# Kernel tuning notes

Hardware: AMD Instinct MI355X
Metric: run time of the kernel (lower is better)

The kernel has to match this reference:

```python
import jax, jax.numpy as jnp
import numpy as np

B, S, D, H = 4, 2048, 1024, 16
HD = D // H

def setup_inputs() -> dict:
    key = jax.random.key(0)
    ks = jax.random.split(key, 5)
    scale = 1.0 / np.sqrt(D)
    x = jax.random.normal(ks[0], (B, S, D), dtype=jnp.float32)
    Wq = jax.random.uniform(ks[1], (D, D), dtype=jnp.float32, minval=-scale, maxval=scale)
    Wk = jax.random.uniform(ks[2], (D, D), dtype=jnp.float32, minval=-scale, maxval=scale)
    Wv = jax.random.uniform(ks[3], (D, D), dtype=jnp.float32, minval=-scale, maxval=scale)
    Wo = jax.random.uniform(ks[4], (D, D), dtype=jnp.float32, minval=-scale, maxval=scale)
    return {"x": x, "Wq": Wq, "Wk": Wk, "Wv": Wv, "Wo": Wo}

def reference(x, Wq, Wk, Wv, Wo):
    # q/k/v: [B,S,D] @ [D,D] -> [B,S,H,HD] -> [B,H,S,HD]
    def heads(w):
        return (x @ w.T).reshape(B, S, H, HD).transpose(0, 2, 1, 3)
    q, k, v = heads(Wq), heads(Wk), heads(Wv)
    scores = jnp.einsum('bhqd,bhkd->bhqk', q, k) / np.sqrt(HD).astype(x.dtype)
    attn = jax.nn.softmax(scores, axis=-1)  # [B,H,S,S]
    out = jnp.einsum('bhqk,bhkd->bhqd', attn, v)
    out = out.transpose(0, 2, 1, 3).reshape(B, S, D)
    return out @ Wo.T
```

## Files before the change

### kernel.cpp

```cpp
#include <hip/hip_runtime.h>

typedef unsigned short u16;
typedef unsigned int u32;
typedef __attribute__((ext_vector_type(8))) __bf16 bf16x8;
typedef __attribute__((ext_vector_type(4))) float f32x4;

#define B_  4
#define S_  2048
#define D_  1024
#define H_  16
#define HD_ 64

#define MFMA __builtin_amdgcn_mfma_f32_16x16x32_bf16


__device__ __forceinline__ u16 f2bf(float f) {
  union { float f; u32 u; } v; v.f = f;
  u32 r = v.u + 0x7fffu + ((v.u >> 16) & 1u);
  return (u16)(r >> 16);
}

__device__ __forceinline__ void gld16(const void* g, void* l) {
  __builtin_amdgcn_global_load_lds((__attribute__((address_space(1))) void*)g,
                                   (__attribute__((address_space(3))) void*)l,
                                   16, 0, 0);
}

__device__ __forceinline__ u32 pack_bf(float lo, float hi) {
  u32 a = __builtin_bit_cast(u32, lo) + 0x8000u;
  u32 b = __builtin_bit_cast(u32, hi) + 0x8000u;
  return __builtin_amdgcn_perm(b, a, 0x07060302u);
}

__global__ __launch_bounds__(256) void cvt_kernel(const float* __restrict__ src,
                                                  u16* __restrict__ dst, int n) {
  int i = (blockIdx.x * 256 + threadIdx.x) * 4;
  if (i + 3 < n) {
    float4 v = *(const float4*)(src + i);
    ushort4 o;
    o.x = f2bf(v.x); o.y = f2bf(v.y); o.z = f2bf(v.z); o.w = f2bf(v.w);
    *(ushort4*)(dst + i) = o;
  }
}

__global__ __launch_bounds__(256) void cvt4_kernel(const float* __restrict__ s0,
                                                   const float* __restrict__ s1,
                                                   const float* __restrict__ s2,
                                                   const float* __restrict__ s3,
                                                   u16* __restrict__ dst) {
  const float* srcs[4] = {s0, s1, s2, s3};
  const float* src = srcs[blockIdx.y];
  u16* d = dst + (size_t)blockIdx.y * (D_ * D_);
  int i = (blockIdx.x * 256 + threadIdx.x) * 4;
  float4 v = *(const float4*)(src + i);
  ushort4 o;
  o.x = f2bf(v.x); o.y = f2bf(v.y); o.z = f2bf(v.z); o.w = f2bf(v.w);
  *(ushort4*)(d + i) = o;
}

__global__ __launch_bounds__(256) void gemm_bt(const u16* __restrict__ A,
                                               const u16* __restrict__ Bm,
                                               u16* __restrict__ Qfp,
                                               u16* __restrict__ Kfp,
                                               u16* __restrict__ Vfp,
                                               float* __restrict__ f32Out,
                                               int mode) {
  __shared__ u16 As[128 * 32];
  __shared__ u16 Bs[128 * 32];
  const int t = threadIdx.x, w = t >> 6, l = t & 63;
  const int lrow = l & 15, quad = l >> 4;
  const int wr = w >> 1, wc = w & 1;
  const int r0 = blockIdx.y * 128, c0 = blockIdx.x * 128;
  const int srow = l >> 2, scol = (l & 3) * 8;

  f32x4 acc[4][4] = {};

  for (int k0 = 0; k0 < 1024; k0 += 32) {
#pragma unroll
    for (int j = 0; j < 2; j++) {
      int rowA = 32 * w + 16 * j + srow;
      gld16(A + (size_t)(r0 + rowA) * 1024 + k0 + scol, &As[(32 * w + 16 * j) * 32]);
      gld16(Bm + (size_t)(c0 + rowA) * 1024 + k0 + scol, &Bs[(32 * w + 16 * j) * 32]);
    }
    __syncthreads();

    bf16x8 af[4], bfr[4];
#pragma unroll
    for (int i = 0; i < 4; i++)
      af[i] = *(const bf16x8*)&As[(64 * wr + 16 * i + lrow) * 32 + 8 * quad];
#pragma unroll
    for (int j = 0; j < 4; j++)
      bfr[j] = *(const bf16x8*)&Bs[(64 * wc + 16 * j + lrow) * 32 + 8 * quad];
#pragma unroll
    for (int i = 0; i < 4; i++)
#pragma unroll
      for (int j = 0; j < 4; j++)
        acc[i][j] = MFMA(af[i], bfr[j], acc[i][j], 0, 0, 0);
    __syncthreads();
  }

  if (mode == 1) {
#pragma unroll
    for (int i = 0; i < 4; i++)
#pragma unroll
      for (int j = 0; j < 4; j++)
#pragma unroll
        for (int rr = 0; rr < 4; rr++) {
          int row = r0 + 64 * wr + 16 * i + 4 * quad + rr;
          int col = c0 + 64 * wc + 16 * j + lrow;
          f32Out[(size_t)row * 1024 + col] = acc[i][j][rr];
        }
    return;
  }

  const int mat = c0 >> 10;
  const int hh = ((c0 & 1023) >> 6) + wc;
  const int bb = r0 >> 11;
  const int S0 = (r0 & 2047) + 64 * wr;
  u16* hb = (mat == 0 ? Qfp : (mat == 1 ? Kfp : Vfp)) +
            (size_t)(bb * 16 + hh) * 131072;

  if (mat < 2) {
    u16* scr = As + w * 1024;
    const int R16 = S0 >> 4;
#pragma unroll
    for (int i = 0; i < 4; i++) {
#pragma unroll
      for (int j = 0; j < 4; j++) {
        int oj = (j >> 1) * 512 + ((2 * j + (lrow >> 3)) & 3) * 128 +
                 quad * 32 + (lrow & 7);
#pragma unroll
        for (int rr = 0; rr < 4; rr++) scr[oj + rr * 8] = f2bf(acc[i][j][rr]);
      }
      uint4 o0 = *(const uint4*)(scr + l * 8);
      uint4 o1 = *(const uint4*)(scr + 512 + l * 8);
      *(uint4*)(hb + (size_t)(R16 + i) * 1024 + l * 8) = o0;
      *(uint4*)(hb + (size_t)(R16 + i) * 1024 + 512 + l * 8) = o1;
    }
  } else {
#pragma unroll
    for (int i = 0; i < 4; i++) {
      int blkr = ((S0 >> 5) + ((4 * i + quad) >> 3)) * 4;
      int lanew = (lrow + 16 * ((2 * i + (quad >> 1)) & 3)) * 8 + 4 * (quad & 1);
#pragma unroll
      for (int j = 0; j < 4; j++) {
        uint2 pw;
        pw.x = pack_bf(acc[i][j][0], acc[i][j][1]);
        pw.y = pack_bf(acc[i][j][2], acc[i][j][3]);
        *(uint2*)(hb + (blkr + j) * 512 + lanew) = pw;
      }
    }
  }
}

__global__ __launch_bounds__(256, 2) void attn_kernel(const u16* __restrict__ Qf,
                                                      const u16* __restrict__ Kf,
                                                      const u16* __restrict__ Vf,
                                                      u16* __restrict__ attnb) {
  __shared__ uint2 Ps[4][2][4][16][4];
  const int t = threadIdx.x, w = t >> 6, l = t & 63;
  const int lrow = l & 15, quad = l >> 4;
  const int f = blockIdx.x;
  const int bh = (f & 7) * 8 + (f >> 7);
  const int qb0 = (f >> 3) & 15;
  const int b = bh >> 4, h = bh & 15;
  const int q0 = qb0 * 128;
  const float C = 0.18033688011f;

  const u16* Qh = Qf + (size_t)bh * 131072;
  const u16* kp = Kf + (size_t)bh * 131072 + l * 8;
  const u16* vp = Vf + (size_t)bh * 131072 + l * 8;

  bf16x8 aq[2][2];
#pragma unroll
  for (int g = 0; g < 2; g++) {
    int qb = qb0 * 8 + 2 * w + g;
#pragma unroll
    for (int st = 0; st < 2; st++)
      aq[g][st] = *(const bf16x8*)(Qh + (qb * 2 + st) * 512 + l * 8);
  }

  float lsum[2] = {0.f, 0.f};
  f32x4 acc[2][4] = {};

  bf16x8 kc[2][4], vc[2][4];
#pragma unroll
  for (int st = 0; st < 2; st++)
#pragma unroll
    for (int nb = 0; nb < 4; nb++) {
      kc[st][nb] = *(const bf16x8*)(kp + (nb * 2 + st) * 512);
      vc[st][nb] = *(const bf16x8*)(vp + (st * 4 + nb) * 512);
    }

#pragma unroll 2
  for (int kt = 0; kt < S_ / 64; kt++) {
    kp += 4096; vp += 4096;
    bf16x8 kn[2][4], vn[2][4];
#pragma unroll
    for (int st = 0; st < 2; st++)
#pragma unroll
      for (int nb = 0; nb < 4; nb++) {
        kn[st][nb] = *(const bf16x8*)(kp + (nb * 2 + st) * 512);
        vn[st][nb] = *(const bf16x8*)(vp + (st * 4 + nb) * 512);
      }

    f32x4 sc[2][4] = {};
#pragma unroll
    for (int st = 0; st < 2; st++)
#pragma unroll
      for (int nb = 0; nb < 4; nb++) {
        sc[0][nb] = MFMA(kc[st][nb], aq[0][st], sc[0][nb], 0, 0, 0);
        sc[1][nb] = MFMA(kc[st][nb], aq[1][st], sc[1][nb], 0, 0, 0);
      }

#pragma unroll
    for (int g = 0; g < 2; g++)
#pragma unroll
      for (int nb = 0; nb < 4; nb++) {
        float p0 = __builtin_amdgcn_exp2f(sc[g][nb][0] * C);
        float p1 = __builtin_amdgcn_exp2f(sc[g][nb][1] * C);
        float p2 = __builtin_amdgcn_exp2f(sc[g][nb][2] * C);
        float p3 = __builtin_amdgcn_exp2f(sc[g][nb][3] * C);
        lsum[g] += (p0 + p1) + (p2 + p3);
        uint2 pw;
        pw.x = pack_bf(p0, p1);
        pw.y = pack_bf(p2, p3);
        Ps[w][g][nb][lrow][quad] = pw;
      }

    bf16x8 pf[2][2];
#pragma unroll
    for (int g = 0; g < 2; g++)
#pragma unroll
      for (int st = 0; st < 2; st++)
        pf[g][st] = *(const bf16x8*)&Ps[w][g][2 * st + (quad >> 1)][lrow][2 * (quad & 1)];

#pragma unroll
    for (int st = 0; st < 2; st++)
#pragma unroll
      for (int nb = 0; nb < 4; nb++) {
        acc[0][nb] = MFMA(pf[0][st], vc[st][nb], acc[0][nb], 0, 0, 0);
        acc[1][nb] = MFMA(pf[1][st], vc[st][nb], acc[1][nb], 0, 0, 0);
      }

#pragma unroll
    for (int st = 0; st < 2; st++)
#pragma unroll
      for (int nb = 0; nb < 4; nb++) {
        kc[st][nb] = kn[st][nb];
        vc[st][nb] = vn[st][nb];
      }
  }

#pragma unroll
  for (int g = 0; g < 2; g++) {
    lsum[g] += __shfl_xor(lsum[g], 16, 64);
    lsum[g] += __shfl_xor(lsum[g], 32, 64);
  }
  float linv[2][4];
#pragma unroll
  for (int g = 0; g < 2; g++)
#pragma unroll
    for (int rr = 0; rr < 4; rr++)
      linv[g][rr] = 1.0f / __shfl(lsum[g], 4 * quad + rr, 64);

#pragma unroll
  for (int g = 0; g < 2; g++)
#pragma unroll
    for (int nb = 0; nb < 4; nb++)
#pragma unroll
      for (int rr = 0; rr < 4; rr++) {
        int q = q0 + 32 * w + 16 * g + 4 * quad + rr;
        int dg = h * HD_ + 16 * nb + lrow;
        attnb[((size_t)b * S_ + q) * (size_t)D_ + dg] = f2bf(acc[g][nb][rr] * linv[g][rr]);
      }
}

extern "C" void kernel_launch(void* const* d_in, const int* in_sizes, int n_in,
                              void* d_out, int out_size, void* d_ws, size_t ws_size,
                              hipStream_t stream) {
  const float* x  = (const float*)d_in[0];
  const float* Wq = (const float*)d_in[1];
  const float* Wk = (const float*)d_in[2];
  const float* Wv = (const float*)d_in[3];
  const float* Wo = (const float*)d_in[4];
  float* out = (float*)d_out;

  const size_t NX = (size_t)B_ * S_ * D_;
  const size_t NW = (size_t)D_ * D_;
  u16* xb    = (u16*)d_ws;
  u16* wall  = xb + NX;
  u16* Qf    = wall + 4 * NW;
  u16* Kf    = Qf + NX;
  u16* Vf    = Kf + NX;
  u16* attnb = Vf + NX;

  cvt_kernel<<<NX / 1024, 256, 0, stream>>>(x, xb, (int)NX);
  cvt4_kernel<<<dim3(NW / 1024, 4), 256, 0, stream>>>(Wq, Wk, Wv, Wo, wall);

  gemm_bt<<<dim3(24, 64), 256, 0, stream>>>(xb, wall, Qf, Kf, Vf, nullptr, 0);

  attn_kernel<<<dim3(1024), 256, 0, stream>>>(Qf, Kf, Vf, attnb);

  gemm_bt<<<dim3(8, 64), 256, 0, stream>>>(attnb, wall + 3 * NW, nullptr, nullptr,
                                           nullptr, out, 1);
}
```

Measured before the change: 303.5 us.

## Halve per-wave query rows in attention to double grid and occupancy

Each wave of the attention kernel now handles one 16-row query group instead of two, so a block covers 64 queries and the grid doubles to 2048 blocks. Launch bounds rise to 4 blocks per CU, and the accumulator, score and LDS buffers are halved to cut register pressure. The cost is that each K/V tile loaded from memory feeds half as many MFMAs, doubling K/V global traffic per query processed. The block-to-(batch,head,query tile) mapping changes to match.

```diff
diff --git a/kernel.cpp b/kernel.cpp
--- a/kernel.cpp
+++ b/kernel.cpp
@@ -153,35 +153,34 @@
   }
 }
 
-__global__ __launch_bounds__(256, 2) void attn_kernel(const u16* __restrict__ Qf,
+__global__ __launch_bounds__(256, 4) void attn_kernel(const u16* __restrict__ Qf,
                                                       const u16* __restrict__ Kf,
                                                       const u16* __restrict__ Vf,
                                                       u16* __restrict__ attnb) {
-  __shared__ uint2 Ps[4][2][4][16][4];
+  __shared__ uint2 Ps[4][4][16][4];
   const int t = threadIdx.x, w = t >> 6, l = t & 63;
   const int lrow = l & 15, quad = l >> 4;
   const int f = blockIdx.x;
-  const int bh = (f & 7) * 8 + (f >> 7);
-  const int qb0 = (f >> 3) & 15;
+  const int bh = (f & 7) + 8 * (f >> 8);
+  const int qt = (f >> 3) & 31;
   const int b = bh >> 4, h = bh & 15;
-  const int q0 = qb0 * 128;
+  const int q0 = qt * 64;
   const float C = 0.18033688011f;
 
   const u16* Qh = Qf + (size_t)bh * 131072;
   const u16* kp = Kf + (size_t)bh * 131072 + l * 8;
   const u16* vp = Vf + (size_t)bh * 131072 + l * 8;
 
-  bf16x8 aq[2][2];
-#pragma unroll
-  for (int g = 0; g < 2; g++) {
-    int qb = qb0 * 8 + 2 * w + g;
-#pragma unroll
-    for (int st = 0; st < 2; st++)
-      aq[g][st] = *(const bf16x8*)(Qh + (qb * 2 + st) * 512 + l * 8);
-  }
-
-  float lsum[2] = {0.f, 0.f};
-  f32x4 acc[2][4] = {};
+  bf16x8 aq[2];
+  {
+    int qb = qt * 4 + w;
+#pragma unroll
+    for (int st = 0; st < 2; st++)
+      aq[st] = *(const bf16x8*)(Qh + (qb * 2 + st) * 512 + l * 8);
+  }
+
+  float lsum = 0.f;
+  f32x4 acc[4] = {};
 
   bf16x8 kc[2][4], vc[2][4];
 #pragma unroll
@@ -204,44 +203,36 @@
         vn[st][nb] = *(const bf16x8*)(vp + (st * 4 + nb) * 512);
       }
 
-    f32x4 sc[2][4] = {};
-#pragma unroll
-    for (int st = 0; st < 2; st++)
-#pragma unroll
-      for (int nb = 0; nb < 4; nb++) {
-        sc[0][nb] = MFMA(kc[st][nb], aq[0][st], sc[0][nb], 0, 0, 0);
-        sc[1][nb] = MFMA(kc[st][nb], aq[1][st], sc[1][nb], 0, 0, 0);
-      }
-
-#pragma unroll
-    for (int g = 0; g < 2; g++)
-#pragma unroll
-      for (int nb = 0; nb < 4; nb++) {
-        float p0 = __builtin_amdgcn_exp2f(sc[g][nb][0] * C);
-        float p1 = __builtin_amdgcn_exp2f(sc[g][nb][1] * C);
-        float p2 = __builtin_amdgcn_exp2f(sc[g][nb][2] * C);
-        float p3 = __builtin_amdgcn_exp2f(sc[g][nb][3] * C);
-        lsum[g] += (p0 + p1) + (p2 + p3);
-        uint2 pw;
-        pw.x = pack_bf(p0, p1);
-        pw.y = pack_bf(p2, p3);
-        Ps[w][g][nb][lrow][quad] = pw;
-      }
-
-    bf16x8 pf[2][2];
-#pragma unroll
-    for (int g = 0; g < 2; g++)
-#pragma unroll
-      for (int st = 0; st < 2; st++)
-        pf[g][st] = *(const bf16x8*)&Ps[w][g][2 * st + (quad >> 1)][lrow][2 * (quad & 1)];
-
-#pragma unroll
-    for (int st = 0; st < 2; st++)
-#pragma unroll
-      for (int nb = 0; nb < 4; nb++) {
-        acc[0][nb] = MFMA(pf[0][st], vc[st][nb], acc[0][nb], 0, 0, 0);
-        acc[1][nb] = MFMA(pf[1][st], vc[st][nb], acc[1][nb], 0, 0, 0);
-      }
+    f32x4 sc[4] = {};
+#pragma unroll
+    for (int st = 0; st < 2; st++)
+#pragma unroll
+      for (int nb = 0; nb < 4; nb++)
+        sc[nb] = MFMA(kc[st][nb], aq[st], sc[nb], 0, 0, 0);
+
+#pragma unroll
+    for (int nb = 0; nb < 4; nb++) {
+      float p0 = __builtin_amdgcn_exp2f(sc[nb][0] * C);
+      float p1 = __builtin_amdgcn_exp2f(sc[nb][1] * C);
+      float p2 = __builtin_amdgcn_exp2f(sc[nb][2] * C);
+      float p3 = __builtin_amdgcn_exp2f(sc[nb][3] * C);
+      lsum += (p0 + p1) + (p2 + p3);
+      uint2 pw;
+      pw.x = pack_bf(p0, p1);
+      pw.y = pack_bf(p2, p3);
+      Ps[w][nb][lrow][quad] = pw;
+    }
+
+    bf16x8 pf[2];
+#pragma unroll
+    for (int st = 0; st < 2; st++)
+      pf[st] = *(const bf16x8*)&Ps[w][2 * st + (quad >> 1)][lrow][2 * (quad & 1)];
+
+#pragma unroll
+    for (int st = 0; st < 2; st++)
+#pragma unroll
+      for (int nb = 0; nb < 4; nb++)
+        acc[nb] = MFMA(pf[st], vc[st][nb], acc[nb], 0, 0, 0);
 
 #pragma unroll
     for (int st = 0; st < 2; st++)
@@ -252,28 +243,21 @@
       }
   }
 
-#pragma unroll
-  for (int g = 0; g < 2; g++) {
-    lsum[g] += __shfl_xor(lsum[g], 16, 64);
-    lsum[g] += __shfl_xor(lsum[g], 32, 64);
-  }
-  float linv[2][4];
-#pragma unroll
-  for (int g = 0; g < 2; g++)
-#pragma unroll
-    for (int rr = 0; rr < 4; rr++)
-      linv[g][rr] = 1.0f / __shfl(lsum[g], 4 * quad + rr, 64);
-
-#pragma unroll
-  for (int g = 0; g < 2; g++)
-#pragma unroll
-    for (int nb = 0; nb < 4; nb++)
-#pragma unroll
-      for (int rr = 0; rr < 4; rr++) {
-        int q = q0 + 32 * w + 16 * g + 4 * quad + rr;
-        int dg = h * HD_ + 16 * nb + lrow;
-        attnb[((size_t)b * S_ + q) * (size_t)D_ + dg] = f2bf(acc[g][nb][rr] * linv[g][rr]);
-      }
+  lsum += __shfl_xor(lsum, 16, 64);
+  lsum += __shfl_xor(lsum, 32, 64);
+  float linv[4];
+#pragma unroll
+  for (int rr = 0; rr < 4; rr++)
+    linv[rr] = 1.0f / __shfl(lsum, 4 * quad + rr, 64);
+
+#pragma unroll
+  for (int nb = 0; nb < 4; nb++)
+#pragma unroll
+    for (int rr = 0; rr < 4; rr++) {
+      int q = q0 + 16 * w + 4 * quad + rr;
+      int dg = h * HD_ + 16 * nb + lrow;
+      attnb[((size_t)b * S_ + q) * (size_t)D_ + dg] = f2bf(acc[nb][rr] * linv[rr]);
+    }
 }
 
 extern "C" void kernel_launch(void* const* d_in, const int* in_sizes, int n_in,
@@ -300,7 +284,7 @@
 
   gemm_bt<<<dim3(24, 64), 256, 0, stream>>>(xb, wall, Qf, Kf, Vf, nullptr, 0);
 
-  attn_kernel<<<dim3(1024), 256, 0, stream>>>(Qf, Kf, Vf, attnb);
+  attn_kernel<<<dim3(2048), 256, 0, stream>>>(Qf, Kf, Vf, attnb);
 
   gemm_bt<<<dim3(8, 64), 256, 0, stream>>>(attnb, wall + 3 * NW, nullptr, nullptr,
                                            nullptr, out, 1);
```

After: 383.0 us. 1.26x slower.
